# Kernel tuning notes

Hardware: AMD Instinct MI355X
Metric: run time of the kernel (lower is better)

## Reference

```python
import jax, jax.numpy as jnp
import numpy as np

M, N, F = 8192, 4096, 1


def quat_to_rotmat(q):
    # q: [N,4] (w,x,y,z) -> [N,3,3]
    q = q / jnp.linalg.norm(q, axis=-1, keepdims=True)
    w, x, y, z = q[:, 0], q[:, 1], q[:, 2], q[:, 3]
    r00 = 1 - 2 * (y * y + z * z)
    r01 = 2 * (x * y - w * z)
    r02 = 2 * (x * z + w * y)
    r10 = 2 * (x * y + w * z)
    r11 = 1 - 2 * (x * x + z * z)
    r12 = 2 * (y * z - w * x)
    r20 = 2 * (x * z - w * y)
    r21 = 2 * (y * z + w * x)
    r22 = 1 - 2 * (x * x + y * y)
    R = jnp.stack([jnp.stack([r00, r01, r02], -1),
                   jnp.stack([r10, r11, r12], -1),
                   jnp.stack([r20, r21, r22], -1)], -2)
    return R


def setup_inputs() -> dict:
    key = jax.random.key(0)
    k1, k2, k3, k4, k5, k6 = jax.random.split(key, 6)
    points = jax.random.normal(k1, (M, 3), dtype=jnp.float32)
    xyz = jax.random.normal(k2, (N, 3), dtype=jnp.float32)
    scale_raw = jax.random.normal(k3, (N, 3), dtype=jnp.float32) * 0.5  # _scale param
    rotation_raw = jax.random.normal(k4, (N, 4), dtype=jnp.float32)     # _rotation param
    opacity_raw = jax.random.normal(k5, (N, 1), dtype=jnp.float32)      # _opacity param
    features = jax.random.normal(k6, (N, F), dtype=jnp.float32)         # _features param
    return {"points": points, "xyz": xyz, "scale_raw": scale_raw,
            "rotation_raw": rotation_raw, "opacity_raw": opacity_raw,
            "features": features}


def reference(points, xyz, scale_raw, rotation_raw, opacity_raw, features):
    scale = jnp.exp(scale_raw)                       # [N,3] activation
    R = quat_to_rotmat(rotation_raw)                 # [N,3,3]
    RS = R * scale[:, None, :]                       # R @ diag(scale)
    cov = jnp.einsum('nik,njk->nij', RS, RS)         # [N,3,3]
    cov_inv = jnp.linalg.inv(cov)                    # [N,3,3]
    diff = points[:, None, :] - xyz[None, :, :]      # [M,N,3]
    mahal = jnp.einsum('mni,nij,mnj->mn', diff, cov_inv, diff)  # [M,N]
    influence = jnp.exp(-0.5 * mahal)                # [M,N]
    opacity = jax.nn.sigmoid(opacity_raw)            # [N,1]
    weights = influence * opacity.T                  # [M,N]
    values = weights @ features                      # [M,F]
    return values, weights
```

## Files before the change

kernel.cpp:

```cpp
#include <hip/hip_runtime.h>


#define THREADS 256
#define JPT 4
#define CHUNKS 4
#define MPB 16
#define NN 4096
#define MM 8192

typedef float f32x4 __attribute__((ext_vector_type(4)));

__global__ __launch_bounds__(THREADS, 2) void gauss_fused(
    const float* __restrict__ points,
    const float* __restrict__ xyz,
    const float* __restrict__ scale_raw,
    const float* __restrict__ rot_raw,
    const float* __restrict__ op_raw,
    const float* __restrict__ feat,
    float* __restrict__ values,
    float* __restrict__ weights) {
  const int t = threadIdx.x;
  const int mbase = blockIdx.x * MPB;

  float A00[CHUNKS][JPT], A01[CHUNKS][JPT], A02[CHUNKS][JPT];
  float A11[CHUNKS][JPT], A12[CHUNKS][JPT], A22[CHUNKS][JPT];
  float B0[CHUNKS][JPT], B1[CHUNKS][JPT], B2[CHUNKS][JPT];
  float CC[CHUNKS][JPT], FF[CHUNKS][JPT];

  const float k = -0.72134752044448170f;

#pragma unroll
  for (int c = 0; c < CHUNKS; ++c) {
    const int nb = c * (NN / CHUNKS) + t * JPT;
    const float4* rot4 = (const float4*)(rot_raw + 4 * (size_t)nb);
    const float4 q0 = rot4[0], q1 = rot4[1], q2 = rot4[2], q3 = rot4[3];
    const float4* sc4 = (const float4*)(scale_raw + 3 * (size_t)nb);
    const float4 s0 = sc4[0], s1 = sc4[1], s2 = sc4[2];
    const float4* xy4 = (const float4*)(xyz + 3 * (size_t)nb);
    const float4 p0 = xy4[0], p1 = xy4[1], p2 = xy4[2];
    const float4 op4 = *(const float4*)(op_raw + nb);
    const float4 f4  = *(const float4*)(feat + nb);

    const float4 q[JPT] = {q0, q1, q2, q3};
    const float sxa[JPT] = {s0.x, s0.w, s1.z, s2.y};
    const float sya[JPT] = {s0.y, s1.x, s1.w, s2.z};
    const float sza[JPT] = {s0.z, s1.y, s2.x, s2.w};
    const float xxa[JPT] = {p0.x, p0.w, p1.z, p2.y};
    const float yya[JPT] = {p0.y, p1.x, p1.w, p2.z};
    const float zza[JPT] = {p0.z, p1.y, p2.x, p2.w};
    const float opa[JPT] = {op4.x, op4.y, op4.z, op4.w};
    const float fa[JPT]  = {f4.x, f4.y, f4.z, f4.w};

#pragma unroll
    for (int j = 0; j < JPT; ++j) {
      float qw = q[j].x, qx = q[j].y, qy = q[j].z, qz = q[j].w;
      const float inorm = rsqrtf(qw*qw + qx*qx + qy*qy + qz*qz);
      qw *= inorm; qx *= inorm; qy *= inorm; qz *= inorm;
      const float sx = __expf(sxa[j]);
      const float sy = __expf(sya[j]);
      const float sz = __expf(sza[j]);
      const float r00 = 1.f - 2.f*(qy*qy + qz*qz);
      const float r01 = 2.f*(qx*qy - qw*qz);
      const float r02 = 2.f*(qx*qz + qw*qy);
      const float r10 = 2.f*(qx*qy + qw*qz);
      const float r11 = 1.f - 2.f*(qx*qx + qz*qz);
      const float r12 = 2.f*(qy*qz - qw*qx);
      const float r20 = 2.f*(qx*qz - qw*qy);
      const float r21 = 2.f*(qy*qz + qw*qx);
      const float r22 = 1.f - 2.f*(qx*qx + qy*qy);
      const float a0 = r00*sx, a1 = r01*sy, a2 = r02*sz;
      const float b0_ = r10*sx, b1_ = r11*sy, b2_ = r12*sz;
      const float c0_ = r20*sx, c1_ = r21*sy, c2_ = r22*sz;
      const float c00 = a0*a0 + a1*a1 + a2*a2;
      const float c01 = a0*b0_ + a1*b1_ + a2*b2_;
      const float c02 = a0*c0_ + a1*c1_ + a2*c2_;
      const float c11 = b0_*b0_ + b1_*b1_ + b2_*b2_;
      const float c12 = b0_*c0_ + b1_*c1_ + b2_*c2_;
      const float c22 = c0_*c0_ + c1_*c1_ + c2_*c2_;
      const float m00 = c11*c22 - c12*c12;
      const float m01 = c02*c12 - c01*c22;
      const float m02 = c01*c12 - c02*c11;
      const float det = c00*m00 + c01*m01 + c02*m02;
      const float idet = 1.f / det;
      const float i00 = m00*idet;
      const float i01 = m01*idet;
      const float i02 = m02*idet;
      const float i11 = (c00*c22 - c02*c02)*idet;
      const float i12 = (c02*c01 - c00*c12)*idet;
      const float i22 = (c00*c11 - c01*c01)*idet;
      const float gx = xxa[j], gy = yya[j], gz = zza[j];
      const float w0 = i00*gx + i01*gy + i02*gz;
      const float w1 = i01*gx + i11*gy + i12*gz;
      const float w2 = i02*gx + i12*gy + i22*gz;
      A00[c][j] = k * i00;
      A11[c][j] = k * i11;
      A22[c][j] = k * i22;
      A01[c][j] = 2.f * k * i01;
      A02[c][j] = 2.f * k * i02;
      A12[c][j] = 2.f * k * i12;
      B0[c][j] = -2.f * k * w0;
      B1[c][j] = -2.f * k * w1;
      B2[c][j] = -2.f * k * w2;
      const float gIg = gx*w0 + gy*w1 + gz*w2;
      const float lop = -__log2f(1.f + __expf(-opa[j]));
      CC[c][j] = k * gIg + lop;
      FF[c][j] = fa[j];
    }
  }

  float vs[MPB];
  const int wv = t >> 6;
  __shared__ float part[MPB][THREADS / 64];

#pragma unroll 2
  for (int i = 0; i < MPB; ++i) {
    const int m = mbase + i;
    const float px = points[3*m+0];
    const float py = points[3*m+1];
    const float pz = points[3*m+2];
    const float pxx = px*px, pyy = py*py, pzz = pz*pz;
    const float pxy = px*py, pxz = px*pz, pyz = py*pz;
    float vsum = 0.f;
#pragma unroll
    for (int c = 0; c < CHUNKS; ++c) {
      f32x4 w;
#pragma unroll
      for (int j = 0; j < JPT; ++j) {
        float arg = CC[c][j];
        arg = fmaf(B2[c][j], pz, arg);
        arg = fmaf(B1[c][j], py, arg);
        arg = fmaf(B0[c][j], px, arg);
        arg = fmaf(A12[c][j], pyz, arg);
        arg = fmaf(A02[c][j], pxz, arg);
        arg = fmaf(A01[c][j], pxy, arg);
        arg = fmaf(A22[c][j], pzz, arg);
        arg = fmaf(A11[c][j], pyy, arg);
        arg = fmaf(A00[c][j], pxx, arg);
        const float wj = __builtin_amdgcn_exp2f(arg);
        w[j] = wj;
        vsum = fmaf(wj, FF[c][j], vsum);
      }
      __builtin_nontemporal_store(
          w, (f32x4*)&weights[(size_t)m * NN + c * (NN / CHUNKS) + t * JPT]);
    }
    vs[i] = vsum;
  }

#pragma unroll
  for (int i = 0; i < MPB; ++i) {
#pragma unroll
    for (int off = 32; off >= 1; off >>= 1)
      vs[i] += __shfl_xor(vs[i], off, 64);
  }
  if ((t & 63) == 0) {
#pragma unroll
    for (int i = 0; i < MPB; ++i) part[i][wv] = vs[i];
  }
  __syncthreads();
  if (t < MPB) {
    values[mbase + t] = (part[t][0] + part[t][1]) + (part[t][2] + part[t][3]);
  }
}

extern "C" void kernel_launch(void* const* d_in, const int* in_sizes, int n_in,
                              void* d_out, int out_size, void* d_ws, size_t ws_size,
                              hipStream_t stream) {
  const float* points    = (const float*)d_in[0];
  const float* xyz       = (const float*)d_in[1];
  const float* scale_raw = (const float*)d_in[2];
  const float* rot_raw   = (const float*)d_in[3];
  const float* op_raw    = (const float*)d_in[4];
  const float* feat      = (const float*)d_in[5];

  float* values  = (float*)d_out;
  float* weights = (float*)d_out + MM;

  gauss_fused<<<MM / MPB, THREADS, 0, stream>>>(
      points, xyz, scale_raw, rot_raw, op_raw, feat, values, weights);
}
```

Baseline: 34.46 us.

## Interchange loops to compute Gaussian params per chunk and stage points in LDS

Swaps the loop nest so each chunk of Gaussian parameters is computed and then used immediately for all points in the block, instead of keeping every chunk's coefficients live in registers. This lowers register pressure, which allows launch bounds of 3 blocks per CU. It also halves points per block, which doubles the number of blocks and doubles the redundant per-Gaussian setup work. Points are staged in shared memory, and the weight stores become regular stores batched four at a time instead of nontemporal stores, which may change cache behaviour for the large weights output.

Result: slower. 44.08 us (+27.9%).

```diff
diff --git a/kernel.cpp b/kernel.cpp
--- a/kernel.cpp
+++ b/kernel.cpp
@@ -3,14 +3,14 @@
 
 #define THREADS 256
 #define JPT 4
-#define CHUNKS 4
-#define MPB 16
+#define MPB 8
 #define NN 4096
 #define MM 8192
+#define CHUNKS (NN / (THREADS * JPT))
 
 typedef float f32x4 __attribute__((ext_vector_type(4)));
 
-__global__ __launch_bounds__(THREADS, 2) void gauss_fused(
+__global__ __launch_bounds__(THREADS, 3) void gauss_fused(
     const float* __restrict__ points,
     const float* __restrict__ xyz,
     const float* __restrict__ scale_raw,
@@ -21,129 +21,135 @@
     float* __restrict__ weights) {
   const int t = threadIdx.x;
   const int mbase = blockIdx.x * MPB;
+  const float k = -0.72134752044448170f;
 
-  float A00[CHUNKS][JPT], A01[CHUNKS][JPT], A02[CHUNKS][JPT];
-  float A11[CHUNKS][JPT], A12[CHUNKS][JPT], A22[CHUNKS][JPT];
-  float B0[CHUNKS][JPT], B1[CHUNKS][JPT], B2[CHUNKS][JPT];
-  float CC[CHUNKS][JPT], FF[CHUNKS][JPT];
+  __shared__ float spts[MPB * 3];
+  __shared__ float part[MPB][THREADS / 64];
+  if (t < MPB * 3) spts[t] = points[mbase * 3 + t];
+  __syncthreads();
 
-  const float k = -0.72134752044448170f;
+  float vs[MPB];
+#pragma unroll
+  for (int i = 0; i < MPB; ++i) vs[i] = 0.f;
 
 #pragma unroll
   for (int c = 0; c < CHUNKS; ++c) {
-    const int nb = c * (NN / CHUNKS) + t * JPT;
-    const float4* rot4 = (const float4*)(rot_raw + 4 * (size_t)nb);
-    const float4 q0 = rot4[0], q1 = rot4[1], q2 = rot4[2], q3 = rot4[3];
-    const float4* sc4 = (const float4*)(scale_raw + 3 * (size_t)nb);
-    const float4 s0 = sc4[0], s1 = sc4[1], s2 = sc4[2];
-    const float4* xy4 = (const float4*)(xyz + 3 * (size_t)nb);
-    const float4 p0 = xy4[0], p1 = xy4[1], p2 = xy4[2];
-    const float4 op4 = *(const float4*)(op_raw + nb);
-    const float4 f4  = *(const float4*)(feat + nb);
+    const int n0 = c * (THREADS * JPT) + t * JPT;
 
-    const float4 q[JPT] = {q0, q1, q2, q3};
-    const float sxa[JPT] = {s0.x, s0.w, s1.z, s2.y};
-    const float sya[JPT] = {s0.y, s1.x, s1.w, s2.z};
-    const float sza[JPT] = {s0.z, s1.y, s2.x, s2.w};
-    const float xxa[JPT] = {p0.x, p0.w, p1.z, p2.y};
-    const float yya[JPT] = {p0.y, p1.x, p1.w, p2.z};
-    const float zza[JPT] = {p0.z, p1.y, p2.x, p2.w};
-    const float opa[JPT] = {op4.x, op4.y, op4.z, op4.w};
-    const float fa[JPT]  = {f4.x, f4.y, f4.z, f4.w};
+    float A00[JPT], A11[JPT], A22[JPT], A01[JPT], A02[JPT], A12[JPT];
+    float B0[JPT], B1[JPT], B2[JPT], CC[JPT], FF[JPT];
+    {
+      const float4* rot4 = (const float4*)(rot_raw + 4 * (size_t)n0);
+      const float4 q0 = rot4[0], q1 = rot4[1], q2 = rot4[2], q3 = rot4[3];
+      const float4* sc4 = (const float4*)(scale_raw + 3 * (size_t)n0);
+      const float4 s0 = sc4[0], s1 = sc4[1], s2 = sc4[2];
+      const float4* xy4 = (const float4*)(xyz + 3 * (size_t)n0);
+      const float4 p0 = xy4[0], p1 = xy4[1], p2 = xy4[2];
+      const float4 op4 = *(const float4*)(op_raw + n0);
+      const float4 f4  = *(const float4*)(feat + n0);
+
+      const float4 q[JPT] = {q0, q1, q2, q3};
+      const float sxa[JPT] = {s0.x, s0.w, s1.z, s2.y};
+      const float sya[JPT] = {s0.y, s1.x, s1.w, s2.z};
+      const float sza[JPT] = {s0.z, s1.y, s2.x, s2.w};
+      const float xxa[JPT] = {p0.x, p0.w, p1.z, p2.y};
+      const float yya[JPT] = {p0.y, p1.x, p1.w, p2.z};
+      const float zza[JPT] = {p0.z, p1.y, p2.x, p2.w};
+      const float opa[JPT] = {op4.x, op4.y, op4.z, op4.w};
+      const float fa[JPT]  = {f4.x, f4.y, f4.z, f4.w};
 
 #pragma unroll
-    for (int j = 0; j < JPT; ++j) {
-      float qw = q[j].x, qx = q[j].y, qy = q[j].z, qz = q[j].w;
-      const float inorm = rsqrtf(qw*qw + qx*qx + qy*qy + qz*qz);
-      qw *= inorm; qx *= inorm; qy *= inorm; qz *= inorm;
-      const float sx = __expf(sxa[j]);
-      const float sy = __expf(sya[j]);
-      const float sz = __expf(sza[j]);
-      const float r00 = 1.f - 2.f*(qy*qy + qz*qz);
-      const float r01 = 2.f*(qx*qy - qw*qz);
-      const float r02 = 2.f*(qx*qz + qw*qy);
-      const float r10 = 2.f*(qx*qy + qw*qz);
-      const float r11 = 1.f - 2.f*(qx*qx + qz*qz);
-      const float r12 = 2.f*(qy*qz - qw*qx);
-      const float r20 = 2.f*(qx*qz - qw*qy);
-      const float r21 = 2.f*(qy*qz + qw*qx);
-      const float r22 = 1.f - 2.f*(qx*qx + qy*qy);
-      const float a0 = r00*sx, a1 = r01*sy, a2 = r02*sz;
-      const float b0_ = r10*sx, b1_ = r11*sy, b2_ = r12*sz;
-      const float c0_ = r20*sx, c1_ = r21*sy, c2_ = r22*sz;
-      const float c00 = a0*a0 + a1*a1 + a2*a2;
-      const float c01 = a0*b0_ + a1*b1_ + a2*b2_;
-      const float c02 = a0*c0_ + a1*c1_ + a2*c2_;
-      const float c11 = b0_*b0_ + b1_*b1_ + b2_*b2_;
-      const float c12 = b0_*c0_ + b1_*c1_ + b2_*c2_;
-      const float c22 = c0_*c0_ + c1_*c1_ + c2_*c2_;
-      const float m00 = c11*c22 - c12*c12;
-      const float m01 = c02*c12 - c01*c22;
-      const float m02 = c01*c12 - c02*c11;
-      const float det = c00*m00 + c01*m01 + c02*m02;
-      const float idet = 1.f / det;
-      const float i00 = m00*idet;
-      const float i01 = m01*idet;
-      const float i02 = m02*idet;
-      const float i11 = (c00*c22 - c02*c02)*idet;
-      const float i12 = (c02*c01 - c00*c12)*idet;
-      const float i22 = (c00*c11 - c01*c01)*idet;
-      const float gx = xxa[j], gy = yya[j], gz = zza[j];
-      const float w0 = i00*gx + i01*gy + i02*gz;
-      const float w1 = i01*gx + i11*gy + i12*gz;
-      const float w2 = i02*gx + i12*gy + i22*gz;
-      A00[c][j] = k * i00;
-      A11[c][j] = k * i11;
-      A22[c][j] = k * i22;
-      A01[c][j] = 2.f * k * i01;
-      A02[c][j] = 2.f * k * i02;
-      A12[c][j] = 2.f * k * i12;
-      B0[c][j] = -2.f * k * w0;
-      B1[c][j] = -2.f * k * w1;
-      B2[c][j] = -2.f * k * w2;
-      const float gIg = gx*w0 + gy*w1 + gz*w2;
-      const float lop = -__log2f(1.f + __expf(-opa[j]));
-      CC[c][j] = k * gIg + lop;
-      FF[c][j] = fa[j];
+      for (int j = 0; j < JPT; ++j) {
+        float qw = q[j].x, qx = q[j].y, qy = q[j].z, qz = q[j].w;
+        const float inorm = rsqrtf(qw*qw + qx*qx + qy*qy + qz*qz);
+        qw *= inorm; qx *= inorm; qy *= inorm; qz *= inorm;
+        const float sx = __expf(sxa[j]);
+        const float sy = __expf(sya[j]);
+        const float sz = __expf(sza[j]);
+        const float r00 = 1.f - 2.f*(qy*qy + qz*qz);
+        const float r01 = 2.f*(qx*qy - qw*qz);
+        const float r02 = 2.f*(qx*qz + qw*qy);
+        const float r10 = 2.f*(qx*qy + qw*qz);
+        const float r11 = 1.f - 2.f*(qx*qx + qz*qz);
+        const float r12 = 2.f*(qy*qz - qw*qx);
+        const float r20 = 2.f*(qx*qz - qw*qy);
+        const float r21 = 2.f*(qy*qz + qw*qx);
+        const float r22 = 1.f - 2.f*(qx*qx + qy*qy);
+        const float a0 = r00*sx, a1 = r01*sy, a2 = r02*sz;
+        const float b0_ = r10*sx, b1_ = r11*sy, b2_ = r12*sz;
+        const float c0_ = r20*sx, c1_ = r21*sy, c2_ = r22*sz;
+        const float c00 = a0*a0 + a1*a1 + a2*a2;
+        const float c01 = a0*b0_ + a1*b1_ + a2*b2_;
+        const float c02 = a0*c0_ + a1*c1_ + a2*c2_;
+        const float c11 = b0_*b0_ + b1_*b1_ + b2_*b2_;
+        const float c12 = b0_*c0_ + b1_*c1_ + b2_*c2_;
+        const float c22 = c0_*c0_ + c1_*c1_ + c2_*c2_;
+        const float m00 = c11*c22 - c12*c12;
+        const float m01 = c02*c12 - c01*c22;
+        const float m02 = c01*c12 - c02*c11;
+        const float det = c00*m00 + c01*m01 + c02*m02;
+        const float idet = 1.f / det;
+        const float i00 = m00*idet;
+        const float i01 = m01*idet;
+        const float i02 = m02*idet;
+        const float i11 = (c00*c22 - c02*c02)*idet;
+        const float i12 = (c02*c01 - c00*c12)*idet;
+        const float i22 = (c00*c11 - c01*c01)*idet;
+        const float gx = xxa[j], gy = yya[j], gz = zza[j];
+        const float w0 = i00*gx + i01*gy + i02*gz;
+        const float w1 = i01*gx + i11*gy + i12*gz;
+        const float w2 = i02*gx + i12*gy + i22*gz;
+        A00[j] = k * i00;
+        A11[j] = k * i11;
+        A22[j] = k * i22;
+        A01[j] = 2.f * k * i01;
+        A02[j] = 2.f * k * i02;
+        A12[j] = 2.f * k * i12;
+        B0[j] = -2.f * k * w0;
+        B1[j] = -2.f * k * w1;
+        B2[j] = -2.f * k * w2;
+        const float gIg = gx*w0 + gy*w1 + gz*w2;
+        const float lop = -__log2f(1.f + __expf(-opa[j]));
+        CC[j] = k * gIg + lop;
+        FF[j] = fa[j];
+      }
     }
-  }
 
-  float vs[MPB];
-  const int wv = t >> 6;
-  __shared__ float part[MPB][THREADS / 64];
-
-#pragma unroll 2
-  for (int i = 0; i < MPB; ++i) {
-    const int m = mbase + i;
-    const float px = points[3*m+0];
-    const float py = points[3*m+1];
-    const float pz = points[3*m+2];
-    const float pxx = px*px, pyy = py*py, pzz = pz*pz;
-    const float pxy = px*py, pxz = px*pz, pyz = py*pz;
-    float vsum = 0.f;
+    f32x4 wbuf[4];
 #pragma unroll
-    for (int c = 0; c < CHUNKS; ++c) {
+    for (int i = 0; i < MPB; ++i) {
+      const float px = spts[3*i+0];
+      const float py = spts[3*i+1];
+      const float pz = spts[3*i+2];
+      const float pxx = px*px, pyy = py*py, pzz = pz*pz;
+      const float pxy = px*py, pxz = px*pz, pyz = py*pz;
       f32x4 w;
+      float vsum = vs[i];
 #pragma unroll
       for (int j = 0; j < JPT; ++j) {
-        float arg = CC[c][j];
-        arg = fmaf(B2[c][j], pz, arg);
-        arg = fmaf(B1[c][j], py, arg);
-        arg = fmaf(B0[c][j], px, arg);
-        arg = fmaf(A12[c][j], pyz, arg);
-        arg = fmaf(A02[c][j], pxz, arg);
-        arg = fmaf(A01[c][j], pxy, arg);
-        arg = fmaf(A22[c][j], pzz, arg);
-        arg = fmaf(A11[c][j], pyy, arg);
-        arg = fmaf(A00[c][j], pxx, arg);
+        float arg = CC[j];
+        arg = fmaf(B2[j], pz, arg);
+        arg = fmaf(B1[j], py, arg);
+        arg = fmaf(B0[j], px, arg);
+        arg = fmaf(A12[j], pyz, arg);
+        arg = fmaf(A02[j], pxz, arg);
+        arg = fmaf(A01[j], pxy, arg);
+        arg = fmaf(A22[j], pzz, arg);
+        arg = fmaf(A11[j], pyy, arg);
+        arg = fmaf(A00[j], pxx, arg);
         const float wj = __builtin_amdgcn_exp2f(arg);
         w[j] = wj;
-        vsum = fmaf(wj, FF[c][j], vsum);
+        vsum = fmaf(wj, FF[j], vsum);
       }
-      __builtin_nontemporal_store(
-          w, (f32x4*)&weights[(size_t)m * NN + c * (NN / CHUNKS) + t * JPT]);
+      vs[i] = vsum;
+      wbuf[i & 3] = w;
+      if ((i & 3) == 3) {
+#pragma unroll
+        for (int b = 0; b < 4; ++b) {
+          *(f32x4*)&weights[(size_t)(mbase + (i - 3 + b)) * NN + n0] = wbuf[b];
+        }
+      }
     }
-    vs[i] = vsum;
   }
 
 #pragma unroll
@@ -152,6 +158,7 @@
     for (int off = 32; off >= 1; off >>= 1)
       vs[i] += __shfl_xor(vs[i], off, 64);
   }
+  const int wv = t >> 6;
   if ((t & 63) == 0) {
 #pragma unroll
     for (int i = 0; i < MPB; ++i) part[i][wv] = vs[i];
```
